# Performance work log

Hardware: AMD Instinct MI355X
Metric: run time of the kernel (lower is better)

Reference implementation:

```python
import jax, jax.numpy as jnp
import numpy as np

COMMITMENT_BETA = 0.25


def setup_inputs() -> dict:
    key = jax.random.key(0)
    k1, k2 = jax.random.split(key)
    B, D, H, W = 32, 256, 32, 32
    NUM_CODES = 1024
    z = jax.random.normal(k1, (B, D, H, W), dtype=jnp.float32)
    codebook = jax.random.normal(k2, (NUM_CODES, D), dtype=jnp.float32)
    return {"z": z, "codebook": codebook}


def reference(z, codebook):
    # z: [B, D, H, W], codebook: [K, D]
    B, D, H, W = z.shape
    z_flat = jnp.transpose(z, (0, 2, 3, 1)).reshape(-1, D)  # [N, D]
    # squared euclidean distances: ||z||^2 - 2 z.W^T + ||W||^2  -> [N, K]
    d = (
        jnp.sum(z_flat * z_flat, axis=1, keepdims=True)
        - 2.0 * (z_flat @ codebook.T)
        + jnp.sum(codebook * codebook, axis=1)[None, :]
    )
    indices = jnp.argmin(d, axis=1)  # [N]
    z_q_flat = codebook[indices]  # [N, D] gather
    # commitment loss: mse(z_flat, stop_grad(z_q_flat))
    diff = z_flat - jax.lax.stop_gradient(z_q_flat)
    commitment_loss = jnp.mean(diff * diff)
    # straight-through estimator
    z_q_flat = z_flat + jax.lax.stop_gradient(z_q_flat - z_flat)
    z_q = jnp.transpose(z_q_flat.reshape(B, H, W, D), (0, 3, 1, 2))
    indices = indices.reshape(B, H, W)
    return z_q, indices, COMMITMENT_BETA * commitment_loss
```

## Files before the change

kernel.cpp:

```cpp
#include <hip/hip_runtime.h>
#include <hip/hip_bf16.h>
#include <hip/hip_fp16.h>

#define DD  256
#define HWD 1024
#define NN  32768
#define KK  1024
#define ZQ_SIZE (NN*DD)
#define IDX_OFF ZQ_SIZE
#define LOSS_OFF (ZQ_SIZE + NN)

#define CBH_OFF    0
#define CNORM_OFF  (KK*DD*2)
#define ROWREC_OFF (CNORM_OFF + KK*4)

#define TH_REFINE 0.2f
#define LOSS_SCALE (0.25f / (float)ZQ_SIZE)

typedef __attribute__((ext_vector_type(8))) _Float16 h16x8;
typedef __attribute__((ext_vector_type(4))) float f32x4;

__device__ __forceinline__ void gload16(const void* g, void* l) {
    __builtin_amdgcn_global_load_lds(
        (const __attribute__((address_space(1))) void*)g,
        (__attribute__((address_space(3))) void*)l, 16, 0, 0);
}

__global__ __launch_bounds__(256)
void vq_prep_kernel(const float* __restrict__ cb, unsigned char* __restrict__ scratch) {
    _Float16* cbh = (_Float16*)(scratch + CBH_OFF);
    float* cn = (float*)(scratch + CNORM_OFF);
    int t = threadIdx.x;
    int row = blockIdx.x * 16 + (t >> 4);
    int dq  = t & 15;
    const float* rp = cb + (size_t)row * DD + dq * 16;
    float nrm = 0.f;
    __attribute__((aligned(16))) _Float16 h[16];
#pragma unroll
    for (int i = 0; i < 4; ++i) {
        float4 v = *(const float4*)(rp + i * 4);
        float xs[4] = {v.x, v.y, v.z, v.w};
#pragma unroll
        for (int j = 0; j < 4; ++j) {
            float x = xs[j];
            h[i * 4 + j] = (_Float16)x;
            nrm = fmaf(x, x, nrm);
        }
    }
    *(uint4*)&cbh[(size_t)row * DD + dq * 16]     = *(uint4*)&h[0];
    *(uint4*)&cbh[(size_t)row * DD + dq * 16 + 8] = *(uint4*)&h[8];
#pragma unroll
    for (int m = 1; m < 16; m <<= 1) nrm += __shfl_xor(nrm, m, 64);
    if (dq == 0) cn[row] = nrm;
}

__global__ __launch_bounds__(256) __attribute__((amdgpu_waves_per_eu(2, 2)))
void vq_mfma_argmin_kernel(const float* __restrict__ z, unsigned char* __restrict__ scratch,
                           float* __restrict__ lossp) {
    const unsigned char* cbh_b = scratch + CBH_OFF;
    const float* cn_g = (const float*)(scratch + CNORM_OFF);
    float* rowrec = (float*)(scratch + ROWREC_OFF);

    __shared__ __attribute__((aligned(16))) short bufs[4 * 8192];
    __shared__ float cn_l[KK];

    const int t    = threadIdx.x;
    const int w    = t >> 6;
    const int lane = t & 63;
    const int ln15 = lane & 15;
    const int lh   = lane >> 4;
    const int g     = w >> 1;
    const int khalf = w & 1;

    const int n0  = blockIdx.x * 64;
    const int b   = n0 >> 10;
    const int hw0 = n0 & 1023;

    const int ksub  = lane >> 5;
    const int chunk = lane & 31;

    const int klr   = khalf * 16 + ln15;
    const int rbase = klr * 256;
    const int rxor  = (klr & 7) << 3;

    *(float4*)&cn_l[t * 4] = *(const float4*)(cn_g + t * 4);

    h16x8 ah[2][8];
    {
        float zsq = 0.f;
        const float* zc = z + (size_t)b * DD * HWD + hw0 + g * 32 + ln15;
#pragma unroll
        for (int nf = 0; nf < 2; ++nf) {
            const float* zp = zc + nf * 16;
#pragma unroll
            for (int ds = 0; ds < 8; ++ds) {
                const int d0 = ds * 32 + lh * 8;
#pragma unroll
                for (int j = 0; j < 8; ++j) {
                    float x = zp[(size_t)(d0 + j) * HWD];
                    ah[nf][ds][j] = (_Float16)x;
                    zsq = fmaf(x, x, zsq);
                }
            }
        }
#pragma unroll
        for (int m = 1; m < 64; m <<= 1) zsq += __shfl_xor(zsq, m, 64);
        if (khalf == 0 && lane == 0) atomicAdd(lossp, zsq * LOSS_SCALE);
    }
    __syncthreads();

    auto STAGE = [&](int tt) {
#pragma unroll
        for (int si = 0; si < 4; ++si) {
            int s  = w * 4 + si;
            int kl = s * 2 + ksub;
            const unsigned char* src = cbh_b
                + (size_t)(tt * 32 + kl) * 512 + ((chunk ^ (kl & 7)) << 4);
            gload16(src, &bufs[(tt & 3) * 8192 + s * 512]);
        }
    };

    float v1[8], k1f[8], v2[8], k2f[8];
#pragma unroll
    for (int s = 0; s < 8; ++s) { v1[s] = 3e38f; v2[s] = 3e38f; k1f[s] = 0.f; k2f[s] = 0.f; }

    auto COMPUTE = [&](int kt) {
        const short* cbt = &bufs[(kt & 3) * 8192];
        const float cnv = cn_l[kt * 32 + klr];
        const float kgf = (float)(kt * 32 + klr);
        f32x4 c0 = {0.f,0.f,0.f,0.f}, c1 = c0, c2 = c0, c3 = c0;
#pragma unroll
        for (int ds = 0; ds < 8; ds += 2) {
            const int ib0 = rbase + (((ds + 0) * 32 + lh * 8) ^ rxor);
            const int ib1 = rbase + (((ds + 1) * 32 + lh * 8) ^ rxor);
            h16x8 b0 = *(const h16x8*)&cbt[ib0];
            h16x8 b1 = *(const h16x8*)&cbt[ib1];
            c0 = __builtin_amdgcn_mfma_f32_16x16x32_f16(ah[0][ds + 0], b0, c0, 0, 0, 0);
            c2 = __builtin_amdgcn_mfma_f32_16x16x32_f16(ah[1][ds + 0], b0, c2, 0, 0, 0);
            c1 = __builtin_amdgcn_mfma_f32_16x16x32_f16(ah[0][ds + 1], b1, c1, 0, 0, 0);
            c3 = __builtin_amdgcn_mfma_f32_16x16x32_f16(ah[1][ds + 1], b1, c3, 0, 0, 0);
        }
        f32x4 s0 = c0 + c1, s1 = c2 + c3;
#pragma unroll
        for (int s = 0; s < 8; ++s) {
            float a = (s < 4) ? s0[s] : s1[s - 4];
            float dist = fmaf(-2.f, a, cnv);
            bool b1c = dist < v1[s];
            bool b2c = dist < v2[s];
            v2[s]  = b1c ? v1[s]  : (b2c ? dist : v2[s]);
            k2f[s] = b1c ? k1f[s] : (b2c ? kgf  : k2f[s]);
            v1[s]  = b1c ? dist : v1[s];
            k1f[s] = b1c ? kgf  : k1f[s];
        }
    };

    STAGE(0); STAGE(1); STAGE(2);

    for (int kt = 0; kt < 29; ++kt) {
        asm volatile("s_waitcnt vmcnt(8)" ::: "memory");
        __builtin_amdgcn_sched_barrier(0);
        __builtin_amdgcn_s_barrier();
        __builtin_amdgcn_sched_barrier(0);
        STAGE(kt + 3);
        COMPUTE(kt);
    }
    asm volatile("s_waitcnt vmcnt(8)" ::: "memory");
    __builtin_amdgcn_sched_barrier(0);
    __builtin_amdgcn_s_barrier();
    __builtin_amdgcn_sched_barrier(0);
    COMPUTE(29);
    asm volatile("s_waitcnt vmcnt(4)" ::: "memory");
    __builtin_amdgcn_sched_barrier(0);
    __builtin_amdgcn_s_barrier();
    __builtin_amdgcn_sched_barrier(0);
    COMPUTE(30);
    asm volatile("s_waitcnt vmcnt(0)" ::: "memory");
    __builtin_amdgcn_sched_barrier(0);
    __builtin_amdgcn_s_barrier();
    __builtin_amdgcn_sched_barrier(0);
    COMPUTE(31);

    __syncthreads();
    float* redv = (float*)bufs;
    float* redk = redv + 64 * 65;
#pragma unroll
    for (int s = 0; s < 8; ++s) {
        int nf = s >> 2, r = s & 3;
        int rowb = g * 32 + nf * 16 + lh * 4 + r;
        redv[klr * 65 + rowb]        = v1[s];
        redk[klr * 65 + rowb]        = k1f[s];
        redv[(32 + klr) * 65 + rowb] = v2[s];
        redk[(32 + klr) * 65 + rowb] = k2f[s];
    }
    __syncthreads();

    const int p = t >> 6, row = t & 63;
    float w1 = 3e38f, w2 = 3e38f, w3 = 3e38f, c1e = 0.f, c2e = 0.f, c3e = 0.f;
#pragma unroll
    for (int q = 0; q < 16; ++q) {
        int i = p * 16 + q;
        float v  = redv[i * 65 + row];
        float kf = redk[i * 65 + row];
        bool lt1 = (v < w1) || (v == w1 && kf < c1e);
        bool lt2 = (v < w2) || (v == w2 && kf < c2e);
        bool lt3 = (v < w3) || (v == w3 && kf < c3e);
        w3 = lt2 ? w2 : (lt3 ? v : w3);  c3e = lt2 ? c2e : (lt3 ? kf : c3e);
        w2 = lt1 ? w1 : (lt2 ? v : w2);  c2e = lt1 ? c1e : (lt2 ? kf : c2e);
        w1 = lt1 ? v : w1;               c1e = lt1 ? kf : c1e;
    }
    __syncthreads();
    {
        float* pv = (float*)bufs;
        float* pk = pv + 4 * 64 * 3;
        int base = (p * 64 + row) * 3;
        pv[base + 0] = w1; pk[base + 0] = c1e;
        pv[base + 1] = w2; pk[base + 1] = c2e;
        pv[base + 2] = w3; pk[base + 2] = c3e;
    }
    __syncthreads();
    if (t < 64) {
        const float* pv = (const float*)bufs;
        const float* pk = pv + 4 * 64 * 3;
        float u1 = 3e38f, u2 = 3e38f, u3 = 3e38f, d1 = 0.f, d2 = 0.f, d3 = 0.f;
#pragma unroll
        for (int i = 0; i < 12; ++i) {
            int pp = i / 3, e = i % 3;
            float v  = pv[(pp * 64 + t) * 3 + e];
            float kf = pk[(pp * 64 + t) * 3 + e];
            bool lt1 = (v < u1) || (v == u1 && kf < d1);
            bool lt2 = (v < u2) || (v == u2 && kf < d2);
            bool lt3 = (v < u3) || (v == u3 && kf < d3);
            u3 = lt2 ? u2 : (lt3 ? v : u3);  d3 = lt2 ? d2 : (lt3 ? kf : d3);
            u2 = lt1 ? u1 : (lt2 ? v : u2);  d2 = lt1 ? d1 : (lt2 ? kf : d2);
            u1 = lt1 ? v : u1;               d1 = lt1 ? kf : d1;
        }
        float4 ra; ra.x = u1; ra.y = d1; ra.z = u2; ra.w = d2;
        float4 rb; rb.x = u3; rb.y = d3; rb.z = 0.f; rb.w = 0.f;
        *(float4*)&rowrec[(size_t)(n0 + t) * 8]     = ra;
        *(float4*)&rowrec[(size_t)(n0 + t) * 8 + 4] = rb;
    }
}

__global__ __launch_bounds__(256)
void vq_refine_kernel(const float* __restrict__ z, const float* __restrict__ cb,
                      const unsigned char* __restrict__ scratch, float* __restrict__ idx_out,
                      float* __restrict__ lossp) {
    const float* rowrec = (const float*)(scratch + ROWREC_OFF);
    const float* cn_g = (const float*)(scratch + CNORM_OFF);
    int n = blockIdx.x * 256 + threadIdx.x;
    int lane = threadIdx.x & 63;
    float4 ra = *(const float4*)&rowrec[(size_t)n * 8];
    float4 rb = *(const float4*)&rowrec[(size_t)n * 8 + 4];
    bool flag = (ra.z - ra.x) <= TH_REFINE;
    float lp = 0.f;
    if (!flag) { idx_out[n] = ra.y; lp = ra.x; }
    unsigned long long mask = __ballot(flag);
    while (mask) {
        int li = __ffsll(mask) - 1;
        mask &= mask - 1;
        int nn  = __shfl(n, li);
        int kk1 = (int)__shfl(ra.y, li);
        int kk2 = (int)__shfl(ra.w, li);
        int kk3 = (int)__shfl(rb.y, li);
        int bb = nn >> 10, hw = nn & 1023;
        const float* zp  = z  + (size_t)bb * DD * HWD + hw;
        const float* c1p = cb + (size_t)kk1 * DD;
        const float* c2p = cb + (size_t)kk2 * DD;
        const float* c3p = cb + (size_t)kk3 * DD;
        float s1 = 0.f, s2 = 0.f, s3 = 0.f;
#pragma unroll
        for (int j = 0; j < 4; ++j) {
            int d = lane + 64 * j;
            float zv = zp[(size_t)d * HWD];
            s1 = fmaf(zv, c1p[d], s1);
            s2 = fmaf(zv, c2p[d], s2);
            s3 = fmaf(zv, c3p[d], s3);
        }
#pragma unroll
        for (int m = 32; m >= 1; m >>= 1) {
            s1 += __shfl_xor(s1, m, 64);
            s2 += __shfl_xor(s2, m, 64);
            s3 += __shfl_xor(s3, m, 64);
        }
        float e1 = cn_g[kk1] - 2.f * s1;
        float e2 = cn_g[kk2] - 2.f * s2;
        float e3 = cn_g[kk3] - 2.f * s3;
        float dch = e1; int kch = kk1;
        if (e2 < dch || (e2 == dch && kk2 < kch)) { dch = e2; kch = kk2; }
        if (e3 < dch || (e3 == dch && kk3 < kch)) { dch = e3; kch = kk3; }
        if (lane == 0) { idx_out[nn] = (float)kch; lp += dch; }
    }
#pragma unroll
    for (int m = 32; m >= 1; m >>= 1) lp += __shfl_xor(lp, m, 64);
    __shared__ float bl[4];
    if (lane == 0) bl[threadIdx.x >> 6] = lp;
    __syncthreads();
    if (threadIdx.x == 0)
        atomicAdd(lossp, (bl[0] + bl[1] + bl[2] + bl[3]) * LOSS_SCALE);
}

__global__ __launch_bounds__(256)
void vq_gather_kernel(const float* __restrict__ cb, float* __restrict__ out) {
    const float* idxf = out + IDX_OFF;
    __shared__ float crow[64][257];
    __shared__ int kidx[64];
    int t = threadIdx.x;
    int w = t >> 6, lane = t & 63;
    int n0 = blockIdx.x * 64;
    int b = n0 >> 10, hw0 = n0 & 1023;
    if (t < 64) kidx[t] = (int)idxf[n0 + t];
    __syncthreads();
    for (int i = 0; i < 16; ++i) {
        int r = w * 16 + i;
        int k = kidx[r];
        float4 v = *(const float4*)(cb + (size_t)k * DD + lane * 4);
        crow[r][lane * 4 + 0] = v.x; crow[r][lane * 4 + 1] = v.y;
        crow[r][lane * 4 + 2] = v.z; crow[r][lane * 4 + 3] = v.w;
    }
    __syncthreads();
    const int zph = t >> 6, hwl = t & 63;
#pragma unroll 4
    for (int dd = 0; dd < 64; ++dd) {
        int d = dd * 4 + zph;
        size_t o = (size_t)b * (DD * HWD) + (size_t)d * HWD + hw0 + hwl;
        out[o] = crow[hwl][d];
    }
}

extern "C" void kernel_launch(void* const* d_in, const int* in_sizes, int n_in,
                              void* d_out, int out_size, void* d_ws, size_t ws_size,
                              hipStream_t stream) {
    const float* z  = (const float*)d_in[0];
    const float* cb = (const float*)d_in[1];
    float* out = (float*)d_out;
    unsigned char* scratch = (unsigned char*)d_out;

    hipMemsetAsync((void*)(out + LOSS_OFF), 0, sizeof(float), stream);

    vq_prep_kernel<<<64, 256, 0, stream>>>(cb, scratch);
    vq_mfma_argmin_kernel<<<512, 256, 0, stream>>>(z, scratch, out + LOSS_OFF);
    vq_refine_kernel<<<128, 256, 0, stream>>>(z, cb, scratch, out + IDX_OFF, out + LOSS_OFF);
    vq_gather_kernel<<<512, 256, 0, stream>>>(cb, out);
}
```

Measured before the change: 80.83 us.

## Split codebook into four ranges per block with fully LDS-resident codes

Restructures the argmin kernel so each 512-thread block handles 256 rows against one quarter of the codebook (256 codes), loading that whole slice into LDS once instead of streaming 32-code tiles through a 4-stage pipeline with barriers per tile. Each wave now owns all code tiles for its own 32 rows, and wave-start offsets are staggered to spread LDS bank usage. The cross-wave LDS top-3 reduction is replaced by shuffle-based merging within the wave, per-range top-3 records go to scratch, and the refine kernel merges the four ranges. The z-squared loss partials are written to scratch and summed in refine rather than through atomics. In exchange, z is re-read by four blocks, LDS use is larger (128KB per block), and the refine kernel reads more record data.

```diff
diff --git a/kernel.cpp b/kernel.cpp
--- a/kernel.cpp
+++ b/kernel.cpp
@@ -10,9 +10,14 @@
 #define IDX_OFF ZQ_SIZE
 #define LOSS_OFF (ZQ_SIZE + NN)
 
+#define RANGES  4
+#define RCODES  256
+#define NTILES  128
+
 #define CBH_OFF    0
 #define CNORM_OFF  (KK*DD*2)
-#define ROWREC_OFF (CNORM_OFF + KK*4)
+#define ZSQ_OFF    (CNORM_OFF + KK*4)
+#define ROWREC_OFF (ZSQ_OFF + 8192)
 
 #define TH_REFINE 0.2f
 #define LOSS_SCALE (0.25f / (float)ZQ_SIZE)
@@ -24,6 +29,14 @@
     __builtin_amdgcn_global_load_lds(
         (const __attribute__((address_space(1))) void*)g,
         (__attribute__((address_space(3))) void*)l, 16, 0, 0);
+}
+
+__device__ __forceinline__ void ins3(float v, float k, float& u1, float& e1,
+                                     float& u2, float& e2, float& u3, float& e3) {
+    bool l1 = v < u1, l2 = v < u2, l3 = v < u3;
+    u3 = l2 ? u2 : (l3 ? v : u3);  e3 = l2 ? e2 : (l3 ? k : e3);
+    u2 = l1 ? u1 : (l2 ? v : u2);  e2 = l1 ? e1 : (l2 ? k : e2);
+    u1 = l1 ? v : u1;              e1 = l1 ? k : e1;
 }
 
 __global__ __launch_bounds__(256)
@@ -54,41 +67,45 @@
     if (dq == 0) cn[row] = nrm;
 }
 
-__global__ __launch_bounds__(256) __attribute__((amdgpu_waves_per_eu(2, 2)))
-void vq_mfma_argmin_kernel(const float* __restrict__ z, unsigned char* __restrict__ scratch,
-                           float* __restrict__ lossp) {
+__global__ __launch_bounds__(512) __attribute__((amdgpu_waves_per_eu(2, 2)))
+void vq_mfma_argmin_kernel(const float* __restrict__ z, unsigned char* __restrict__ scratch) {
     const unsigned char* cbh_b = scratch + CBH_OFF;
     const float* cn_g = (const float*)(scratch + CNORM_OFF);
+    float* zsqp = (float*)(scratch + ZSQ_OFF);
     float* rowrec = (float*)(scratch + ROWREC_OFF);
 
-    __shared__ __attribute__((aligned(16))) short bufs[4 * 8192];
-    __shared__ float cn_l[KK];
+    __shared__ __attribute__((aligned(16))) short cbuf[RCODES * 256];
+    __shared__ float cn_l[RCODES];
 
     const int t    = threadIdx.x;
     const int w    = t >> 6;
     const int lane = t & 63;
     const int ln15 = lane & 15;
     const int lh   = lane >> 4;
-    const int g     = w >> 1;
-    const int khalf = w & 1;
-
-    const int n0  = blockIdx.x * 64;
-    const int b   = n0 >> 10;
-    const int hw0 = n0 & 1023;
+
+    const int bid   = blockIdx.x;
+    const int range = bid & 3;
+    const int tile  = bid >> 2;
+    const int n0    = tile * 256;
+    const int b     = n0 >> 10;
+    const int hw0   = n0 & 1023;
 
     const int ksub  = lane >> 5;
     const int chunk = lane & 31;
-
-    const int klr   = khalf * 16 + ln15;
-    const int rbase = klr * 256;
-    const int rxor  = (klr & 7) << 3;
-
-    *(float4*)&cn_l[t * 4] = *(const float4*)(cn_g + t * 4);
+#pragma unroll
+    for (int i = 0; i < 16; ++i) {
+        int slice = w * 16 + i;
+        int kl = slice * 2 + ksub;
+        const unsigned char* src = cbh_b
+            + (size_t)(range * RCODES + kl) * 512 + ((chunk ^ (kl & 7)) << 4);
+        gload16(src, &cbuf[slice * 512]);
+    }
+    if (t < RCODES) cn_l[t] = cn_g[range * RCODES + t];
 
     h16x8 ah[2][8];
     {
         float zsq = 0.f;
-        const float* zc = z + (size_t)b * DD * HWD + hw0 + g * 32 + ln15;
+        const float* zc = z + (size_t)b * DD * HWD + hw0 + w * 32 + ln15;
 #pragma unroll
         for (int nf = 0; nf < 2; ++nf) {
             const float* zp = zc + nf * 16;
@@ -105,36 +122,30 @@
         }
 #pragma unroll
         for (int m = 1; m < 64; m <<= 1) zsq += __shfl_xor(zsq, m, 64);
-        if (khalf == 0 && lane == 0) atomicAdd(lossp, zsq * LOSS_SCALE);
+        if (range == 0 && lane == 0) zsqp[tile * 8 + w] = zsq;
     }
     __syncthreads();
 
-    auto STAGE = [&](int tt) {
-#pragma unroll
-        for (int si = 0; si < 4; ++si) {
-            int s  = w * 4 + si;
-            int kl = s * 2 + ksub;
-            const unsigned char* src = cbh_b
-                + (size_t)(tt * 32 + kl) * 512 + ((chunk ^ (kl & 7)) << 4);
-            gload16(src, &bufs[(tt & 3) * 8192 + s * 512]);
-        }
-    };
-
     float v1[8], k1f[8], v2[8], k2f[8];
 #pragma unroll
     for (int s = 0; s < 8; ++s) { v1[s] = 3e38f; v2[s] = 3e38f; k1f[s] = 0.f; k2f[s] = 0.f; }
 
-    auto COMPUTE = [&](int kt) {
-        const short* cbt = &bufs[(kt & 3) * 8192];
-        const float cnv = cn_l[kt * 32 + klr];
-        const float kgf = (float)(kt * 32 + klr);
+    const int kstart = (w * 2) & 15;
+    for (int it = 0; it < 16; ++it) {
+        const int kt  = (it + kstart) & 15;
+        const int klr = kt * 16 + ln15;
+        const float cnv = cn_l[klr];
+        const float kgf = (float)(range * RCODES + klr);
+        const int rbase = klr * 256;
+        const int rxor  = (klr & 7) << 3;
+
         f32x4 c0 = {0.f,0.f,0.f,0.f}, c1 = c0, c2 = c0, c3 = c0;
 #pragma unroll
         for (int ds = 0; ds < 8; ds += 2) {
             const int ib0 = rbase + (((ds + 0) * 32 + lh * 8) ^ rxor);
             const int ib1 = rbase + (((ds + 1) * 32 + lh * 8) ^ rxor);
-            h16x8 b0 = *(const h16x8*)&cbt[ib0];
-            h16x8 b1 = *(const h16x8*)&cbt[ib1];
+            h16x8 b0 = *(const h16x8*)&cbuf[ib0];
+            h16x8 b1 = *(const h16x8*)&cbuf[ib1];
             c0 = __builtin_amdgcn_mfma_f32_16x16x32_f16(ah[0][ds + 0], b0, c0, 0, 0, 0);
             c2 = __builtin_amdgcn_mfma_f32_16x16x32_f16(ah[1][ds + 0], b0, c2, 0, 0, 0);
             c1 = __builtin_amdgcn_mfma_f32_16x16x32_f16(ah[0][ds + 1], b1, c1, 0, 0, 0);
@@ -152,92 +163,37 @@
             v1[s]  = b1c ? dist : v1[s];
             k1f[s] = b1c ? kgf  : k1f[s];
         }
-    };
-
-    STAGE(0); STAGE(1); STAGE(2);
-
-    for (int kt = 0; kt < 29; ++kt) {
-        asm volatile("s_waitcnt vmcnt(8)" ::: "memory");
-        __builtin_amdgcn_sched_barrier(0);
-        __builtin_amdgcn_s_barrier();
-        __builtin_amdgcn_sched_barrier(0);
-        STAGE(kt + 3);
-        COMPUTE(kt);
-    }
-    asm volatile("s_waitcnt vmcnt(8)" ::: "memory");
-    __builtin_amdgcn_sched_barrier(0);
-    __builtin_amdgcn_s_barrier();
-    __builtin_amdgcn_sched_barrier(0);
-    COMPUTE(29);
-    asm volatile("s_waitcnt vmcnt(4)" ::: "memory");
-    __builtin_amdgcn_sched_barrier(0);
-    __builtin_amdgcn_s_barrier();
-    __builtin_amdgcn_sched_barrier(0);
-    COMPUTE(30);
-    asm volatile("s_waitcnt vmcnt(0)" ::: "memory");
-    __builtin_amdgcn_sched_barrier(0);
-    __builtin_amdgcn_s_barrier();
-    __builtin_amdgcn_sched_barrier(0);
-    COMPUTE(31);
-
-    __syncthreads();
-    float* redv = (float*)bufs;
-    float* redk = redv + 64 * 65;
-#pragma unroll
-    for (int s = 0; s < 8; ++s) {
-        int nf = s >> 2, r = s & 3;
-        int rowb = g * 32 + nf * 16 + lh * 4 + r;
-        redv[klr * 65 + rowb]        = v1[s];
-        redk[klr * 65 + rowb]        = k1f[s];
-        redv[(32 + klr) * 65 + rowb] = v2[s];
-        redk[(32 + klr) * 65 + rowb] = k2f[s];
-    }
-    __syncthreads();
-
-    const int p = t >> 6, row = t & 63;
-    float w1 = 3e38f, w2 = 3e38f, w3 = 3e38f, c1e = 0.f, c2e = 0.f, c3e = 0.f;
-#pragma unroll
-    for (int q = 0; q < 16; ++q) {
-        int i = p * 16 + q;
-        float v  = redv[i * 65 + row];
-        float kf = redk[i * 65 + row];
-        bool lt1 = (v < w1) || (v == w1 && kf < c1e);
-        bool lt2 = (v < w2) || (v == w2 && kf < c2e);
-        bool lt3 = (v < w3) || (v == w3 && kf < c3e);
-        w3 = lt2 ? w2 : (lt3 ? v : w3);  c3e = lt2 ? c2e : (lt3 ? kf : c3e);
-        w2 = lt1 ? w1 : (lt2 ? v : w2);  c2e = lt1 ? c1e : (lt2 ? kf : c2e);
-        w1 = lt1 ? v : w1;               c1e = lt1 ? kf : c1e;
-    }
-    __syncthreads();
-    {
-        float* pv = (float*)bufs;
-        float* pk = pv + 4 * 64 * 3;
-        int base = (p * 64 + row) * 3;
-        pv[base + 0] = w1; pk[base + 0] = c1e;
-        pv[base + 1] = w2; pk[base + 1] = c2e;
-        pv[base + 2] = w3; pk[base + 2] = c3e;
-    }
-    __syncthreads();
-    if (t < 64) {
-        const float* pv = (const float*)bufs;
-        const float* pk = pv + 4 * 64 * 3;
-        float u1 = 3e38f, u2 = 3e38f, u3 = 3e38f, d1 = 0.f, d2 = 0.f, d3 = 0.f;
-#pragma unroll
-        for (int i = 0; i < 12; ++i) {
-            int pp = i / 3, e = i % 3;
-            float v  = pv[(pp * 64 + t) * 3 + e];
-            float kf = pk[(pp * 64 + t) * 3 + e];
-            bool lt1 = (v < u1) || (v == u1 && kf < d1);
-            bool lt2 = (v < u2) || (v == u2 && kf < d2);
-            bool lt3 = (v < u3) || (v == u3 && kf < d3);
-            u3 = lt2 ? u2 : (lt3 ? v : u3);  d3 = lt2 ? d2 : (lt3 ? kf : d3);
-            u2 = lt1 ? u1 : (lt2 ? v : u2);  d2 = lt1 ? d1 : (lt2 ? kf : d2);
-            u1 = lt1 ? v : u1;               d1 = lt1 ? kf : d1;
-        }
-        float4 ra; ra.x = u1; ra.y = d1; ra.z = u2; ra.w = d2;
-        float4 rb; rb.x = u3; rb.y = d3; rb.z = 0.f; rb.w = 0.f;
-        *(float4*)&rowrec[(size_t)(n0 + t) * 8]     = ra;
-        *(float4*)&rowrec[(size_t)(n0 + t) * 8 + 4] = rb;
+    }
+
+    float u3[8], e3[8];
+#pragma unroll
+    for (int s = 0; s < 8; ++s) { u3[s] = 3e38f; e3[s] = 0.f; }
+#pragma unroll
+    for (int m = 1; m < 16; m <<= 1) {
+#pragma unroll
+        for (int s = 0; s < 8; ++s) {
+            float o1 = __shfl_xor(v1[s],  m, 64);
+            float p1 = __shfl_xor(k1f[s], m, 64);
+            float o2 = __shfl_xor(v2[s],  m, 64);
+            float p2 = __shfl_xor(k2f[s], m, 64);
+            float o3 = __shfl_xor(u3[s],  m, 64);
+            float p3 = __shfl_xor(e3[s],  m, 64);
+            ins3(o1, p1, v1[s], k1f[s], v2[s], k2f[s], u3[s], e3[s]);
+            ins3(o2, p2, v1[s], k1f[s], v2[s], k2f[s], u3[s], e3[s]);
+            ins3(o3, p3, v1[s], k1f[s], v2[s], k2f[s], u3[s], e3[s]);
+        }
+    }
+    if (ln15 == 0) {
+#pragma unroll
+        for (int s = 0; s < 8; ++s) {
+            int nf = s >> 2, r = s & 3;
+            int rowl = w * 32 + nf * 16 + lh * 4 + r;
+            size_t base = ((size_t)range * NN + n0 + rowl) * 8;
+            float4 ra; ra.x = v1[s]; ra.y = k1f[s]; ra.z = v2[s]; ra.w = k2f[s];
+            float4 rb; rb.x = u3[s]; rb.y = e3[s];  rb.z = 0.f;   rb.w = 0.f;
+            *(float4*)&rowrec[base]     = ra;
+            *(float4*)&rowrec[base + 4] = rb;
+        }
     }
 }
 
@@ -247,21 +203,33 @@
                       float* __restrict__ lossp) {
     const float* rowrec = (const float*)(scratch + ROWREC_OFF);
     const float* cn_g = (const float*)(scratch + CNORM_OFF);
+    const float* zsqp = (const float*)(scratch + ZSQ_OFF);
     int n = blockIdx.x * 256 + threadIdx.x;
     int lane = threadIdx.x & 63;
-    float4 ra = *(const float4*)&rowrec[(size_t)n * 8];
-    float4 rb = *(const float4*)&rowrec[(size_t)n * 8 + 4];
-    bool flag = (ra.z - ra.x) <= TH_REFINE;
+
+    float u1 = 3e38f, u2 = 3e38f, u3 = 3e38f, e1 = 0.f, e2 = 0.f, e3 = 0.f;
+#pragma unroll
+    for (int r = 0; r < RANGES; ++r) {
+        size_t base = ((size_t)r * NN + n) * 8;
+        float4 ra = *(const float4*)&rowrec[base];
+        float4 rb = *(const float4*)&rowrec[base + 4];
+        ins3(ra.x, ra.y, u1, e1, u2, e2, u3, e3);
+        ins3(ra.z, ra.w, u1, e1, u2, e2, u3, e3);
+        ins3(rb.x, rb.y, u1, e1, u2, e2, u3, e3);
+    }
+
+    bool flag = (u2 - u1) <= TH_REFINE;
     float lp = 0.f;
-    if (!flag) { idx_out[n] = ra.y; lp = ra.x; }
+    if (!flag) { idx_out[n] = e1; lp = u1; }
+
     unsigned long long mask = __ballot(flag);
     while (mask) {
         int li = __ffsll(mask) - 1;
         mask &= mask - 1;
         int nn  = __shfl(n, li);
-        int kk1 = (int)__shfl(ra.y, li);
-        int kk2 = (int)__shfl(ra.w, li);
-        int kk3 = (int)__shfl(rb.y, li);
+        int kk1 = (int)__shfl(e1, li);
+        int kk2 = (int)__shfl(e2, li);
+        int kk3 = (int)__shfl(e3, li);
         int bb = nn >> 10, hw = nn & 1023;
         const float* zp  = z  + (size_t)bb * DD * HWD + hw;
         const float* c1p = cb + (size_t)kk1 * DD;
@@ -282,14 +250,20 @@
             s2 += __shfl_xor(s2, m, 64);
             s3 += __shfl_xor(s3, m, 64);
         }
-        float e1 = cn_g[kk1] - 2.f * s1;
-        float e2 = cn_g[kk2] - 2.f * s2;
-        float e3 = cn_g[kk3] - 2.f * s3;
-        float dch = e1; int kch = kk1;
-        if (e2 < dch || (e2 == dch && kk2 < kch)) { dch = e2; kch = kk2; }
-        if (e3 < dch || (e3 == dch && kk3 < kch)) { dch = e3; kch = kk3; }
+        float d1 = cn_g[kk1] - 2.f * s1;
+        float d2 = cn_g[kk2] - 2.f * s2;
+        float d3 = cn_g[kk3] - 2.f * s3;
+        float dch = d1; int kch = kk1;
+        if (d2 < dch || (d2 == dch && kk2 < kch)) { dch = d2; kch = kk2; }
+        if (d3 < dch || (d3 == dch && kk3 < kch)) { dch = d3; kch = kk3; }
         if (lane == 0) { idx_out[nn] = (float)kch; lp += dch; }
     }
+
+    if (blockIdx.x == 0) {
+        const float4 zv = *(const float4*)&zsqp[threadIdx.x * 4];
+        lp += (zv.x + zv.y) + (zv.z + zv.w);
+    }
+
 #pragma unroll
     for (int m = 32; m >= 1; m >>= 1) lp += __shfl_xor(lp, m, 64);
     __shared__ float bl[4];
@@ -338,7 +312,7 @@
     hipMemsetAsync((void*)(out + LOSS_OFF), 0, sizeof(float), stream);
 
     vq_prep_kernel<<<64, 256, 0, stream>>>(cb, scratch);
-    vq_mfma_argmin_kernel<<<512, 256, 0, stream>>>(z, scratch, out + LOSS_OFF);
+    vq_mfma_argmin_kernel<<<512, 512, 0, stream>>>(z, scratch);
     vq_refine_kernel<<<128, 256, 0, stream>>>(z, cb, scratch, out + IDX_OFF, out + LOSS_OFF);
     vq_gather_kernel<<<512, 256, 0, stream>>>(cb, out);
 }
```

Result: slower. 103.7 us (+28.3%).

## Stage z tile through LDS with coalesced float4 loads and drop loss atomics

Applied to the files above, without the earlier changes.

The argmin kernel used to load z with strided scalar loads (one element per lane per d, each wave covering only 16 contiguous hw positions) while also converting to fp16 in registers. It now has all 256 threads load z with coalesced float4 reads, write fp16 into a swizzled LDS tile, and then read the MFMA A fragments from LDS. The per-block z-squared sum is written to a scratch slot instead of atomically added to the loss, and the refine kernel folds those partials into its own reduction. This removes redundant global reads, since both k-halves previously loaded z, and removes one atomic per block, at the cost of an extra LDS round trip and a barrier.

```diff
diff --git a/kernel.cpp b/kernel.cpp
--- a/kernel.cpp
+++ b/kernel.cpp
@@ -12,7 +12,8 @@
 
 #define CBH_OFF    0
 #define CNORM_OFF  (KK*DD*2)
-#define ROWREC_OFF (CNORM_OFF + KK*4)
+#define ZSQ_OFF    (CNORM_OFF + KK*4)
+#define ROWREC_OFF (ZSQ_OFF + 2048)
 
 #define TH_REFINE 0.2f
 #define LOSS_SCALE (0.25f / (float)ZQ_SIZE)
@@ -24,6 +25,10 @@
     __builtin_amdgcn_global_load_lds(
         (const __attribute__((address_space(1))) void*)g,
         (__attribute__((address_space(3))) void*)l, 16, 0, 0);
+}
+__device__ __forceinline__ short f16bits(float x) {
+    _Float16 h = (_Float16)x;
+    return *reinterpret_cast<short*>(&h);
 }
 
 __global__ __launch_bounds__(256)
@@ -55,14 +60,15 @@
 }
 
 __global__ __launch_bounds__(256) __attribute__((amdgpu_waves_per_eu(2, 2)))
-void vq_mfma_argmin_kernel(const float* __restrict__ z, unsigned char* __restrict__ scratch,
-                           float* __restrict__ lossp) {
+void vq_mfma_argmin_kernel(const float* __restrict__ z, unsigned char* __restrict__ scratch) {
     const unsigned char* cbh_b = scratch + CBH_OFF;
     const float* cn_g = (const float*)(scratch + CNORM_OFF);
+    float* zsqp = (float*)(scratch + ZSQ_OFF);
     float* rowrec = (float*)(scratch + ROWREC_OFF);
 
     __shared__ __attribute__((aligned(16))) short bufs[4 * 8192];
     __shared__ float cn_l[KK];
+    __shared__ float zred[4];
 
     const int t    = threadIdx.x;
     const int w    = t >> 6;
@@ -85,28 +91,42 @@
 
     *(float4*)&cn_l[t * 4] = *(const float4*)(cn_g + t * 4);
 
+    {
+        short* zlds = bufs;
+        const int zd = t >> 4;
+        const int zq = t & 15;
+        const float* zb = z + (size_t)b * DD * HWD + hw0 + zq * 4;
+        float zsq = 0.f;
+#pragma unroll
+        for (int p = 0; p < 16; ++p) {
+            int d = p * 16 + zd;
+            float4 v = *(const float4*)(zb + (size_t)d * HWD);
+            zsq = fmaf(v.x, v.x, zsq); zsq = fmaf(v.y, v.y, zsq);
+            zsq = fmaf(v.z, v.z, zsq); zsq = fmaf(v.w, v.w, zsq);
+            float xs[4] = {v.x, v.y, v.z, v.w};
+#pragma unroll
+            for (int i = 0; i < 4; ++i) {
+                int row = zq * 4 + i;
+                zlds[row * 256 + (d ^ ((row & 15) << 3))] = f16bits(xs[i]);
+            }
+        }
+#pragma unroll
+        for (int m = 1; m < 64; m <<= 1) zsq += __shfl_xor(zsq, m, 64);
+        if (lane == 0) zred[w] = zsq;
+    }
+    __syncthreads();
+
     h16x8 ah[2][8];
-    {
-        float zsq = 0.f;
-        const float* zc = z + (size_t)b * DD * HWD + hw0 + g * 32 + ln15;
-#pragma unroll
-        for (int nf = 0; nf < 2; ++nf) {
-            const float* zp = zc + nf * 16;
-#pragma unroll
-            for (int ds = 0; ds < 8; ++ds) {
-                const int d0 = ds * 32 + lh * 8;
-#pragma unroll
-                for (int j = 0; j < 8; ++j) {
-                    float x = zp[(size_t)(d0 + j) * HWD];
-                    ah[nf][ds][j] = (_Float16)x;
-                    zsq = fmaf(x, x, zsq);
-                }
-            }
-        }
-#pragma unroll
-        for (int m = 1; m < 64; m <<= 1) zsq += __shfl_xor(zsq, m, 64);
-        if (khalf == 0 && lane == 0) atomicAdd(lossp, zsq * LOSS_SCALE);
-    }
+#pragma unroll
+    for (int nf = 0; nf < 2; ++nf) {
+#pragma unroll
+        for (int ds = 0; ds < 8; ++ds) {
+            int row = g * 32 + nf * 16 + ln15;
+            int d0  = ds * 32 + lh * 8;
+            ah[nf][ds] = *(const h16x8*)&bufs[row * 256 + (d0 ^ ((row & 15) << 3))];
+        }
+    }
+    if (t == 0) zsqp[blockIdx.x] = (zred[0] + zred[1]) + (zred[2] + zred[3]);
     __syncthreads();
 
     auto STAGE = [&](int tt) {
@@ -247,6 +267,7 @@
                       float* __restrict__ lossp) {
     const float* rowrec = (const float*)(scratch + ROWREC_OFF);
     const float* cn_g = (const float*)(scratch + CNORM_OFF);
+    const float* zsqp = (const float*)(scratch + ZSQ_OFF);
     int n = blockIdx.x * 256 + threadIdx.x;
     int lane = threadIdx.x & 63;
     float4 ra = *(const float4*)&rowrec[(size_t)n * 8];
@@ -290,6 +311,10 @@
         if (e3 < dch || (e3 == dch && kk3 < kch)) { dch = e3; kch = kk3; }
         if (lane == 0) { idx_out[nn] = (float)kch; lp += dch; }
     }
+    if (blockIdx.x == 0) {
+        const float2 zv = *(const float2*)&zsqp[threadIdx.x * 2];
+        lp += zv.x + zv.y;
+    }
 #pragma unroll
     for (int m = 32; m >= 1; m >>= 1) lp += __shfl_xor(lp, m, 64);
     __shared__ float bl[4];
@@ -338,7 +363,7 @@
     hipMemsetAsync((void*)(out + LOSS_OFF), 0, sizeof(float), stream);
 
     vq_prep_kernel<<<64, 256, 0, stream>>>(cb, scratch);
-    vq_mfma_argmin_kernel<<<512, 256, 0, stream>>>(z, scratch, out + LOSS_OFF);
+    vq_mfma_argmin_kernel<<<512, 256, 0, stream>>>(z, scratch);
     vq_refine_kernel<<<128, 256, 0, stream>>>(z, cb, scratch, out + IDX_OFF, out + LOSS_OFF);
     vq_gather_kernel<<<512, 256, 0, stream>>>(cb, out);
 }
```

Measured after the change: 70.15 us. 1.15x faster.
